# Performance work log

Measured on AMD Instinct MI355X. Metric: run time of the kernel, lower is better.

The kernel has to match this reference:

```python
import jax, jax.numpy as jnp
import numpy as np

EPS = 1e-8


def l2norm(x, axis):
    # matches torch: x / (sqrt(sum(x^2)) + eps)
    return x / (jnp.sqrt(jnp.sum(x * x, axis=axis, keepdims=True)) + EPS)


def setup_inputs() -> dict:
    key = jax.random.key(0)
    k1, k2, k3, k4, k5 = jax.random.split(key, 5)
    I, C, L, R, D = 16, 32, 32, 36, 1024  # n_image, n_caption, max_words, n_regions, embed_dim
    img_emb = l2norm(jax.random.normal(k1, (I, R, D), jnp.float32), -1)
    cap_emb = l2norm(jax.random.normal(k2, (C, L, D), jnp.float32), -1)
    W_emb = jax.random.normal(k3, (D, D), jnp.float32)  # nn.Embedding weight, N(0,1) default init
    sim_map_w = 2.5 + 0.1 * jax.random.normal(k4, (1, D), jnp.float32)  # init_weight: normal(2.5, 0.1)
    temp_scale_w = jnp.full((1, 1), np.log(1.0 / 0.07), jnp.float32)    # init_weight
    temp_learnable_w = jnp.full((1, 1), 4.0, jnp.float32)               # init_weight
    cap_lens = jax.random.randint(k5, (C,), 4, L + 1, jnp.int32)        # ragged caption lengths in [4, L]
    return dict(img_emb=img_emb, cap_emb=cap_emb, W_emb=W_emb, sim_map_w=sim_map_w,
                temp_scale_w=temp_scale_w, temp_learnable_w=temp_learnable_w, cap_lens=cap_lens)


def reference(img_emb, cap_emb, W_emb, sim_map_w, temp_scale_w, temp_learnable_w, cap_lens):
    D = W_emb.shape[0]
    L = cap_emb.shape[1]
    # --- dimension-weight branch (caption-independent) ---
    # linspace(0, D, D).long(): last index is D (out of range in torch); gather with clip.
    idx = jnp.floor(jnp.linspace(0.0, D, D)).astype(jnp.int32)
    weights = jax.nn.sigmoid(jnp.take(W_emb, idx, axis=0, mode='clip'))  # (D, D)
    mean_p = jnp.mean(weights, axis=1)                  # (D,)
    std_p = jnp.std(weights, axis=1, ddof=1)            # torch.std is unbiased
    thres = mean_p + sim_map_w[0] * std_p               # (D,)
    values = jnp.exp(temp_learnable_w[0, 0]) * (weights - thres[:, None])
    mask_p = jnp.tanh(jnp.exp(values))
    Dlw = l2norm(mask_p * weights, axis=1)              # Dim_learned_weights (D, D)
    diag = Dlw.sum(0)                                   # Diagonal (D,); diag_embed matmul == elementwise scale
    smooth = jnp.exp(temp_scale_w[0, 0])
    # --- vectorized ragged per-caption cross attention ---
    wmask = (jnp.arange(L)[None, :] < cap_lens[:, None]).astype(cap_emb.dtype)  # (C, L)
    # attn[c,i,l,r] = tanh(sum_d cap[c,l,d] * diag[d] * img[i,r,d])
    attn = jnp.tanh(jnp.einsum('cld,ird->cilr', cap_emb, img_emb * diag))
    attn = jnp.where(attn >= 0, attn, 0.1 * attn) * wmask[:, None, :, None]  # LeakyReLU(0.1), zero padded words
    attn = attn / (jnp.sqrt(jnp.sum(attn * attn, axis=2, keepdims=True)) + EPS)  # l2norm over word dim
    attn = jax.nn.softmax(attn * smooth, axis=3)        # softmax over regions
    ctx = l2norm(jnp.einsum('cilr,ird->cild', attn, img_emb), axis=-1)  # Context_img
    sim_loc = ctx * cap_emb[:, None, :, :]
    sim_sub = jnp.einsum('cild,ed->cile', sim_loc, Dlw)  # sim_loc @ Dlw.T
    sim_vec = l2norm(sim_sub, axis=-1).sum(-1)           # (C, I, L)
    # mean over the n_word valid words of each caption
    sim = jnp.sum(sim_vec * wmask[:, None, :], axis=2) / cap_lens[:, None].astype(cap_emb.dtype)  # (C, I)
    return sim.T  # (n_image, n_caption), matching torch.cat(sim_all, 1)
```

## Files before the change

kernel.cpp:

```cpp
#include <hip/hip_runtime.h>
#include <hip/hip_bf16.h>

#define I_N 16
#define C_N 32
#define L_N 32
#define R_N 36
#define D_N 1024
#define EPSF 1e-8f

typedef _Float16 f16;
typedef __attribute__((ext_vector_type(8))) _Float16 half8;
typedef __attribute__((ext_vector_type(4))) float floatx4;

__device__ __forceinline__ void gl16(const f16* g, f16* l) {
  __builtin_amdgcn_global_load_lds(
      (const __attribute__((address_space(1))) void*)g,
      (__attribute__((address_space(3))) void*)l, 16, 0, 0);
}

__device__ __forceinline__ float fast_tanh(float x) {
  float q = __expf(-2.f * fabsf(x));
  float t = (1.f - q) / (1.f + q);
  return (x >= 0.f) ? t : -t;
}

__device__ __forceinline__ float wave_sum64(float v) {
  #pragma unroll
  for (int off = 32; off > 0; off >>= 1) v += __shfl_xor(v, off, 64);
  return v;
}

__global__ __launch_bounds__(256) void k_dlw(const float* __restrict__ W,
    const float* __restrict__ simw, const float* __restrict__ tlw,
    const float* __restrict__ img,
    f16* __restrict__ DlwH, f16* __restrict__ imgP) {
  int gw = blockIdx.x * 4 + (threadIdx.x >> 6);
  int lane = threadIdx.x & 63;
  if (gw >= 1024) {
    int row = gw - 1024;
    int i = row / 48, r = row % 48;
    size_t dst = (size_t)row * D_N;
    #pragma unroll
    for (int q = 0; q < 4; ++q) {
      int col = lane * 4 + q * 256;
      f16 h4[4];
      if (r < R_N) {
        size_t src = ((size_t)i * R_N + r) * D_N;
        float4 v = *(const float4*)(img + src + col);
        h4[0] = (f16)v.x; h4[1] = (f16)v.y; h4[2] = (f16)v.z; h4[3] = (f16)v.w;
      } else {
        h4[0] = h4[1] = h4[2] = h4[3] = (f16)0.f;
      }
      *(float2*)(imgP + dst + col) = *(float2*)h4;
    }
    return;
  }
  int row = gw;
  const float* Wr = W + (size_t)row * D_N;
  float w[16]; float p = 0.f;
  #pragma unroll
  for (int q = 0; q < 4; ++q) {
    float4 v = *(const float4*)(Wr + lane * 4 + q * 256);
    w[q*4+0] = 1.f / (1.f + __expf(-v.x));
    w[q*4+1] = 1.f / (1.f + __expf(-v.y));
    w[q*4+2] = 1.f / (1.f + __expf(-v.z));
    w[q*4+3] = 1.f / (1.f + __expf(-v.w));
    p += w[q*4+0] + w[q*4+1] + w[q*4+2] + w[q*4+3];
  }
  float S = wave_sum64(p);
  float mean = S * (1.f / 1024.f);
  p = 0.f;
  #pragma unroll
  for (int k = 0; k < 16; ++k) { float d = w[k] - mean; p += d * d; }
  float S2 = wave_sum64(p);
  float stdv = sqrtf(S2 * (1.f / 1023.f));
  float thres = mean + simw[row] * stdv;
  float eT = __expf(tlw[0]);
  p = 0.f;
  #pragma unroll
  for (int k = 0; k < 16; ++k) {
    float y = __expf(eT * (w[k] - thres));
    float q2 = __expf(-2.f * y);
    float mp = (1.f - q2) / (1.f + q2);
    w[k] = mp * w[k];
    p += w[k] * w[k];
  }
  float S3 = wave_sum64(p);
  float inv = 1.f / (sqrtf(S3) + EPSF);
  #pragma unroll
  for (int q = 0; q < 4; ++q) {
    f16 h4[4];
    #pragma unroll
    for (int t = 0; t < 4; ++t) h4[t] = (f16)(w[q*4+t] * inv);
    *(float2*)(DlwH + (size_t)row * D_N + lane * 4 + q * 256) = *(float2*)h4;
  }
}

__global__ __launch_bounds__(256) void k_dpp(const f16* __restrict__ DlwH,
    const int* __restrict__ lens, float* __restrict__ dpart,
    int* __restrict__ pfx, int* __restrict__ mp) {
  int bid = blockIdx.x;
  if (bid < 64) {
    int p = bid >> 2;
    int col = (bid & 3) * 256 + threadIdx.x;
    float s = 0.f;
    #pragma unroll 8
    for (int r = p * 64; r < p * 64 + 64; ++r) s += (float)DlwH[(size_t)r * D_N + col];
    dpart[(size_t)p * D_N + col] = s;
  } else if (threadIdx.x < 64) {
    int l = threadIdx.x;
    int v = (l < 32) ? lens[l] : 0;
    int s = v;
    #pragma unroll
    for (int off = 1; off < 32; off <<= 1) {
      int t = __shfl_up(s, off, 64);
      if (l >= off) s += t;
    }
    if (l < 32) pfx[l] = s - v;
    if (l == 31) { pfx[32] = s; mp[0] = s * 16; }
  }
}

__global__ __launch_bounds__(256) void k_capd(const float* __restrict__ dpart,
    const float* __restrict__ cap, f16* __restrict__ capD) {
  __shared__ float dg[D_N];
  int tid = threadIdx.x;
  #pragma unroll
  for (int k = 0; k < 4; ++k) {
    int col = tid + k * 256;
    float s = 0.f;
    #pragma unroll
    for (int p = 0; p < 16; ++p) s += dpart[(size_t)p * D_N + col];
    dg[col] = s;
  }
  __syncthreads();
  size_t base = (size_t)blockIdx.x * D_N;
  #pragma unroll
  for (int k = 0; k < 4; ++k) {
    int j = tid + k * 256;
    capD[base + j] = (f16)(cap[base + j] * dg[j]);
  }
}

__global__ __launch_bounds__(256) void k_qk(const f16* __restrict__ A,
    const f16* __restrict__ B, const int* __restrict__ lens,
    const float* __restrict__ tsw, float* __restrict__ pw) {
  int mt = blockIdx.x;
  int i  = blockIdx.y;
  int tid = threadIdx.x;
  int w = tid >> 6, lane = tid & 63;
  int l15 = lane & 15, h = lane >> 4;
  __shared__ __align__(16) f16 Als[64 * 32];
  __shared__ __align__(16) f16 Bls[48 * 32];
  __shared__ float att[64][49];
  __shared__ float cn[2][R_N];
  floatx4 acc[3];
  #pragma unroll
  for (int nf = 0; nf < 3; ++nf) acc[nf] = (floatx4)0.f;
  int arow = tid >> 2;
  int u = tid & 3;
  int vf = (u | ((arow & 1) << 2)) ^ ((arow >> 1) & 7);
  int wofs = (((arow & 62) | (vf >> 2)) * 32) + (vf & 3) * 8;
  const f16* Ag = A + (size_t)(mt * 64 + arow) * D_N + u * 8;
  const f16* Bg = B + (size_t)(i * 48 + arow) * D_N + u * 8;
  int v2 = (h | ((l15 & 1) << 2)) ^ ((l15 >> 1) & 7);
  int rbit = (v2 >> 2) & 1;
  int pun = (v2 & 3) * 8;
  int aoff = (w * 16 + (l15 & 14) + rbit) * 32 + pun;
  int boff[3];
  #pragma unroll
  for (int nf = 0; nf < 3; ++nf) boff[nf] = (nf * 16 + (l15 & 14) + rbit) * 32 + pun;
  for (int kk = 0; kk < D_N; kk += 32) {
    *(float4*)(&Als[wofs]) = *(const float4*)(Ag + kk);
    if (tid < 192) *(float4*)(&Bls[wofs]) = *(const float4*)(Bg + kk);
    __syncthreads();
    half8 a = *(const half8*)(&Als[aoff]);
    #pragma unroll
    for (int nf = 0; nf < 3; ++nf) {
      half8 b = *(const half8*)(&Bls[boff[nf]]);
      acc[nf] = __builtin_amdgcn_mfma_f32_16x16x32_f16(a, b, acc[nf], 0, 0, 0);
    }
    __syncthreads();
  }
  int len0 = lens[mt * 2], len1 = lens[mt * 2 + 1];
  #pragma unroll
  for (int nf = 0; nf < 3; ++nf)
    #pragma unroll
    for (int j = 0; j < 4; ++j) {
      int ml = w * 16 + h * 4 + j;
      int n = nf * 16 + l15;
      float t = fast_tanh(acc[nf][j]);
      float v = (t >= 0.f) ? t : 0.1f * t;
      int len = (ml >= 32) ? len1 : len0;
      if ((ml & 31) >= len || n >= R_N) v = 0.f;
      att[ml][n] = v;
    }
  __syncthreads();
  for (int e = tid; e < 2 * R_N; e += 256) {
    int cc = e / R_N, r = e % R_N;
    float s = 0.f;
    #pragma unroll
    for (int l = 0; l < 32; ++l) { float a = att[cc * 32 + l][r]; s += a * a; }
    cn[cc][r] = sqrtf(s) + EPSF;
  }
  __syncthreads();
  if (tid < 64) {
    int cc = tid >> 5, l = tid & 31;
    float smooth = __expf(tsw[0]);
    float mx = -3.4e38f;
    #pragma unroll
    for (int r = 0; r < R_N; ++r) {
      float z = att[tid][r] / cn[cc][r] * smooth;
      att[tid][r] = z;
      mx = fmaxf(mx, z);
    }
    float se = 0.f;
    #pragma unroll
    for (int r = 0; r < R_N; ++r) {
      float e2 = __expf(att[tid][r] - mx);
      att[tid][r] = e2;
      se += e2;
    }
    float inv = 1.f / se;
    float* dst = pw + ((size_t)i * 1024 + (mt * 2 + cc) * 32 + l) * R_N;
    #pragma unroll
    for (int r = 0; r < R_N; ++r) dst[r] = att[tid][r] * inv;
  }
}

__global__ __launch_bounds__(256) void k_ctx(const float* __restrict__ pw,
    const f16* __restrict__ imgP, const float* __restrict__ cap,
    const int* __restrict__ lens, const int* __restrict__ pfx,
    f16* __restrict__ slc) {
  int c  = blockIdx.x;
  int i  = blockIdx.y;
  int tid = threadIdx.x;
  int w = tid >> 6;
  int cg = tid & 63;
  int len = lens[c];
  int pf = pfx[c];
  __shared__ float pA[32][R_N];
  __shared__ __align__(16) f16 rows[R_N][1024];
  for (int e = tid; e < 32 * R_N; e += 256) {
    int rr = e / R_N, r = e % R_N;
    pA[rr][r] = pw[((size_t)i * 1024 + c * 32 + rr) * R_N + r];
  }
  const f16* base = imgP + (size_t)i * 48 * D_N;
  #pragma unroll
  for (int t = 0; t < 9; ++t) {
    int rr = w * 9 + t;
    const f16* src = base + (size_t)rr * D_N + cg * 8;
    gl16(src,       &rows[rr][0]);
    gl16(src + 512, &rows[rr][512]);
  }
  __syncthreads();
  int d0 = cg * 8, d1 = 512 + cg * 8;
  #pragma unroll
  for (int sub = 0; sub < 2; ++sub) {
    float acc[4][16];
    #pragma unroll
    for (int j = 0; j < 4; ++j)
      #pragma unroll
      for (int q = 0; q < 16; ++q) acc[j][q] = 0.f;
    for (int k = 0; k < R_N; ++k) {
      half8 h0 = *(const half8*)(&rows[k][d0]);
      half8 h1 = *(const half8*)(&rows[k][d1]);
      float bv[16];
      #pragma unroll
      for (int q = 0; q < 8; ++q) { bv[q] = (float)h0[q]; bv[8 + q] = (float)h1[q]; }
      #pragma unroll
      for (int j = 0; j < 4; ++j) {
        float a = pA[sub * 16 + w * 4 + j][k];
        #pragma unroll
        for (int q = 0; q < 16; ++q) acc[j][q] += a * bv[q];
      }
    }
    #pragma unroll
    for (int j = 0; j < 4; ++j) {
      int l = sub * 16 + w * 4 + j;
      float ss = 0.f;
      #pragma unroll
      for (int q = 0; q < 16; ++q) ss += acc[j][q] * acc[j][q];
      #pragma unroll
      for (int off = 1; off < 64; off <<= 1) ss += __shfl_xor(ss, off, 64);
      if (l < len) {
        float inv = 1.f / (sqrtf(ss) + EPSF);
        const float* capr = cap + ((size_t)c * L_N + l) * D_N;
        float4 c0 = *(const float4*)(capr + d0);
        float4 c1 = *(const float4*)(capr + d0 + 4);
        float4 c2 = *(const float4*)(capr + d1);
        float4 c3 = *(const float4*)(capr + d1 + 4);
        float cv[16] = {c0.x,c0.y,c0.z,c0.w, c1.x,c1.y,c1.z,c1.w,
                        c2.x,c2.y,c2.z,c2.w, c3.x,c3.y,c3.z,c3.w};
        union { f16 h[16]; float4 f4[2]; } u;
        #pragma unroll
        for (int q = 0; q < 16; ++q) u.h[q] = (f16)(acc[j][q] * inv * cv[q]);
        f16* dst = slc + ((size_t)((pf + l) * 16 + i)) * D_N;
        *(float4*)(dst + d0) = u.f4[0];
        *(float4*)(dst + d1) = u.f4[1];
      }
    }
  }
}

__global__ __launch_bounds__(256) void k_gemm(const f16* __restrict__ A,
    const f16* __restrict__ B, const int* __restrict__ mp,
    float* __restrict__ rs16, float* __restrict__ rq16) {
  int bx = blockIdx.x, by = blockIdx.y;
  int Mp = mp[0];
  int m0 = bx * 128, n0 = by * 128;
  if (m0 >= Mp) return;
  int tid = threadIdx.x;
  int w = tid >> 6, lane = tid & 63;
  int l15 = lane & 15, h = lane >> 4;
  int wm = w >> 1, wn = w & 1;
  __shared__ __align__(16) f16 AB[3][2][128 * 32];
  floatx4 acc[4][4];
  #pragma unroll
  for (int mf = 0; mf < 4; ++mf)
    #pragma unroll
    for (int nf = 0; nf < 4; ++nf) acc[mf][nf] = (floatx4)0.f;

  int r_p = lane >> 2, u_p = lane & 3;
  int sw = (r_p >> 1) & 7;
  int val = (u_p | ((r_p & 1) << 2)) ^ sw;
  int r_l = (r_p & 14) | (val >> 2);
  int u_l = val & 3;
  const f16* As0 = A + (size_t)(m0 + w * 32 +  0 + r_l) * D_N + u_l * 8;
  const f16* As1 = A + (size_t)(m0 + w * 32 + 16 + r_l) * D_N + u_l * 8;
  const f16* Bs0 = B + (size_t)(n0 + w * 32 +  0 + r_l) * D_N + u_l * 8;
  const f16* Bs1 = B + (size_t)(n0 + w * 32 + 16 + r_l) * D_N + u_l * 8;

  int v2 = (h | ((l15 & 1) << 2)) ^ ((l15 >> 1) & 7);
  int rbit = (v2 >> 2) & 1;
  int pun = (v2 & 3) * 8;
  int aoff[4], boff[4];
  #pragma unroll
  for (int f = 0; f < 4; ++f) {
    aoff[f] = (wm * 64 + f * 16 + (l15 & 14) + rbit) * 32 + pun;
    boff[f] = (wn * 64 + f * 16 + (l15 & 14) + rbit) * 32 + pun;
  }

  #define STAGE(kt, b) { \
    int kof = (kt) * 32; \
    gl16(As0 + kof, &AB[b][0][(w * 32 +  0) * 32]); \
    gl16(As1 + kof, &AB[b][0][(w * 32 + 16) * 32]); \
    gl16(Bs0 + kof, &AB[b][1][(w * 32 +  0) * 32]); \
    gl16(Bs1 + kof, &AB[b][1][(w * 32 + 16) * 32]); }

  #define COMPUTE(b) { \
    half8 af[4], bf[4]; \
    _Pragma("unroll") for (int f = 0; f < 4; ++f) af[f] = *(const half8*)(&AB[b][0][aoff[f]]); \
    _Pragma("unroll") for (int f = 0; f < 4; ++f) bf[f] = *(const half8*)(&AB[b][1][boff[f]]); \
    _Pragma("unroll") for (int mf = 0; mf < 4; ++mf) \
      _Pragma("unroll") for (int nf = 0; nf < 4; ++nf) \
        acc[mf][nf] = __builtin_amdgcn_mfma_f32_16x16x32_f16(af[mf], bf[nf], acc[mf][nf], 0, 0, 0); }

  STAGE(0, 0);
  STAGE(1, 1);
  int cur = 0, n2 = 2;
  for (int kk = 0; kk < 30; ++kk) {
    STAGE(kk + 2, n2);
    asm volatile("s_waitcnt vmcnt(8)" ::: "memory");
    __builtin_amdgcn_s_barrier();
    __builtin_amdgcn_sched_barrier(0);
    COMPUTE(cur);
    __builtin_amdgcn_s_barrier();
    cur = (cur == 2) ? 0 : cur + 1;
    n2  = (n2  == 2) ? 0 : n2  + 1;
  }
  asm volatile("s_waitcnt vmcnt(4)" ::: "memory");
  __builtin_amdgcn_s_barrier();
  __builtin_amdgcn_sched_barrier(0);
  COMPUTE(cur);
  __builtin_amdgcn_s_barrier();
  cur = (cur == 2) ? 0 : cur + 1;
  asm volatile("s_waitcnt vmcnt(0)" ::: "memory");
  __builtin_amdgcn_s_barrier();
  __builtin_amdgcn_sched_barrier(0);
  COMPUTE(cur);
  #undef STAGE
  #undef COMPUTE

  int slot = by * 2 + wn;
  #pragma unroll
  for (int mf = 0; mf < 4; ++mf)
    #pragma unroll
    for (int j = 0; j < 4; ++j) {
      float s = 0.f, q = 0.f;
      #pragma unroll
      for (int nf = 0; nf < 4; ++nf) { float v = acc[mf][nf][j]; s += v; q += v * v; }
      #pragma unroll
      for (int off = 1; off < 16; off <<= 1) { s += __shfl_xor(s, off, 64); q += __shfl_xor(q, off, 64); }
      if (l15 == 0) {
        int m = m0 + wm * 64 + mf * 16 + h * 4 + j;
        rs16[(size_t)slot * 16384 + m] = s;
        rq16[(size_t)slot * 16384 + m] = q;
      }
    }
}

__global__ __launch_bounds__(64) void k_final(const float* __restrict__ rs16,
    const float* __restrict__ rq16, const int* __restrict__ lens,
    const int* __restrict__ pfx, float* __restrict__ out) {
  int b = blockIdx.x;
  int c = b & 31;
  int l = threadIdx.x;
  int len = lens[c];
  float sv = 0.f;
  if (l < len) {
    int i = b >> 5;
    int row = (pfx[c] + l) * 16 + i;
    float rs = 0.f, rq = 0.f;
    #pragma unroll
    for (int s = 0; s < 16; ++s) {
      rs += rs16[(size_t)s * 16384 + row];
      rq += rq16[(size_t)s * 16384 + row];
    }
    sv = rs / (sqrtf(rq) + EPSF);
  }
  #pragma unroll
  for (int off = 32; off > 0; off >>= 1) sv += __shfl_down(sv, off, 64);
  if (l == 0) out[b] = sv / (float)len;
}

extern "C" void kernel_launch(void* const* d_in, const int* in_sizes, int n_in,
                              void* d_out, int out_size, void* d_ws, size_t ws_size,
                              hipStream_t stream) {
  const float* img  = (const float*)d_in[0];
  const float* cap  = (const float*)d_in[1];
  const float* W    = (const float*)d_in[2];
  const float* simw = (const float*)d_in[3];
  const float* tsw  = (const float*)d_in[4];
  const float* tlw  = (const float*)d_in[5];
  const int*   lens = (const int*)d_in[6];
  float* out = (float*)d_out;

  char* wsB = (char*)d_ws;
  if (ws_size < 51122176) return;
  f16*   DlwH  = (f16*)  (wsB + 4194304);
  f16*   capD  = (f16*)  (wsB + 6295552);
  f16*   imgP  = (f16*)  (wsB + 8392704);
  float* dpart = (float*)(wsB + 9965568);
  int*   mp    = (int*)  (wsB + 10031104);
  int*   pfx   = (int*)  (wsB + 10031360);
  float* pw    = (float*)(wsB + 13111296);
  f16*   slc   = (f16*)  (wsB + 15470592);
  float* rs16  = (float*)(wsB + 49025024);
  float* rq16  = (float*)(wsB + 50073600);

  k_dlw<<<448, 256, 0, stream>>>(W, simw, tlw, img, DlwH, imgP);
  k_dpp<<<65, 256, 0, stream>>>(DlwH, lens, dpart, pfx, mp);
  k_capd<<<1024, 256, 0, stream>>>(dpart, cap, capD);
  k_qk<<<dim3(16, 16), 256, 0, stream>>>(capD, imgP, lens, tsw, pw);
  k_ctx<<<dim3(32, 16), 256, 0, stream>>>(pw, imgP, cap, lens, pfx, slc);
  k_gemm<<<dim3(128, 8), 256, 0, stream>>>(slc, DlwH, mp, rs16, rq16);
  k_final<<<512, 64, 0, stream>>>(rs16, rq16, lens, pfx, out);
}
```

Baseline: 101.3 us.

## Pipeline QK GEMM loads with triple-buffered direct-to-LDS async copies

Replaces the synchronous global-to-register-to-LDS staging in the QK kernel with global_load_lds async copies into a three-stage ring buffer. Explicit vmcnt waits and barriers let loads for future k-tiles overlap with the MFMA compute on the current tile. This is meant to hide global memory latency in the K loop. Each warp now loads 16 rows of B too, so B rows beyond the needed 48 are fetched, which adds redundant traffic and may read past the buffer end. LDS usage also grows.

```diff
diff --git a/kernel.cpp b/kernel.cpp
--- a/kernel.cpp
+++ b/kernel.cpp
@@ -150,19 +150,22 @@
   int tid = threadIdx.x;
   int w = tid >> 6, lane = tid & 63;
   int l15 = lane & 15, h = lane >> 4;
-  __shared__ __align__(16) f16 Als[64 * 32];
-  __shared__ __align__(16) f16 Bls[48 * 32];
+  __shared__ __align__(16) f16 Abuf[3][64 * 32];
+  __shared__ __align__(16) f16 Bbuf[3][64 * 32];
   __shared__ float att[64][49];
   __shared__ float cn[2][R_N];
   floatx4 acc[3];
   #pragma unroll
   for (int nf = 0; nf < 3; ++nf) acc[nf] = (floatx4)0.f;
-  int arow = tid >> 2;
-  int u = tid & 3;
-  int vf = (u | ((arow & 1) << 2)) ^ ((arow >> 1) & 7);
-  int wofs = (((arow & 62) | (vf >> 2)) * 32) + (vf & 3) * 8;
-  const f16* Ag = A + (size_t)(mt * 64 + arow) * D_N + u * 8;
-  const f16* Bg = B + (size_t)(i * 48 + arow) * D_N + u * 8;
+
+  int r_p = lane >> 2, u_p = lane & 3;
+  int sw = (r_p >> 1) & 7;
+  int val = (u_p | ((r_p & 1) << 2)) ^ sw;
+  int r_l = (r_p & 14) | (val >> 2);
+  int u_l = val & 3;
+  const f16* Ag = A + (size_t)(mt * 64 + w * 16 + r_l) * D_N + u_l * 8;
+  const f16* Bg = B + (size_t)(i * 48 + w * 16 + r_l) * D_N + u_l * 8;
+
   int v2 = (h | ((l15 & 1) << 2)) ^ ((l15 >> 1) & 7);
   int rbit = (v2 >> 2) & 1;
   int pun = (v2 & 3) * 8;
@@ -170,18 +173,43 @@
   int boff[3];
   #pragma unroll
   for (int nf = 0; nf < 3; ++nf) boff[nf] = (nf * 16 + (l15 & 14) + rbit) * 32 + pun;
-  for (int kk = 0; kk < D_N; kk += 32) {
-    *(float4*)(&Als[wofs]) = *(const float4*)(Ag + kk);
-    if (tid < 192) *(float4*)(&Bls[wofs]) = *(const float4*)(Bg + kk);
-    __syncthreads();
-    half8 a = *(const half8*)(&Als[aoff]);
-    #pragma unroll
-    for (int nf = 0; nf < 3; ++nf) {
-      half8 b = *(const half8*)(&Bls[boff[nf]]);
-      acc[nf] = __builtin_amdgcn_mfma_f32_16x16x32_f16(a, b, acc[nf], 0, 0, 0);
-    }
-    __syncthreads();
-  }
+
+  #define QSTAGE(kt, b) { \
+    int kof = (kt) * 32; \
+    gl16(Ag + kof, &Abuf[b][(w * 16) * 32]); \
+    gl16(Bg + kof, &Bbuf[b][(w * 16) * 32]); }
+  #define QCOMPUTE(b) { \
+    half8 a = *(const half8*)(&Abuf[b][aoff]); \
+    _Pragma("unroll") for (int nf = 0; nf < 3; ++nf) { \
+      half8 bb = *(const half8*)(&Bbuf[b][boff[nf]]); \
+      acc[nf] = __builtin_amdgcn_mfma_f32_16x16x32_f16(a, bb, acc[nf], 0, 0, 0); } }
+
+  QSTAGE(0, 0);
+  QSTAGE(1, 1);
+  int cur = 0, n2 = 2;
+  for (int kk = 0; kk < 30; ++kk) {
+    QSTAGE(kk + 2, n2);
+    asm volatile("s_waitcnt vmcnt(4)" ::: "memory");
+    __builtin_amdgcn_s_barrier();
+    __builtin_amdgcn_sched_barrier(0);
+    QCOMPUTE(cur);
+    __builtin_amdgcn_s_barrier();
+    cur = (cur == 2) ? 0 : cur + 1;
+    n2  = (n2  == 2) ? 0 : n2  + 1;
+  }
+  asm volatile("s_waitcnt vmcnt(2)" ::: "memory");
+  __builtin_amdgcn_s_barrier();
+  __builtin_amdgcn_sched_barrier(0);
+  QCOMPUTE(cur);
+  __builtin_amdgcn_s_barrier();
+  cur = (cur == 2) ? 0 : cur + 1;
+  asm volatile("s_waitcnt vmcnt(0)" ::: "memory");
+  __builtin_amdgcn_s_barrier();
+  __builtin_amdgcn_sched_barrier(0);
+  QCOMPUTE(cur);
+  #undef QSTAGE
+  #undef QCOMPUTE
+
   int len0 = lens[mt * 2], len1 = lens[mt * 2 + 1];
   #pragma unroll
   for (int nf = 0; nf < 3; ++nf)
```

New measurement: 94.14 us. 7.0% less time.
